# Kernel optimization log

Hardware: AMD Instinct MI355X
Metric: run time of the kernel (lower is better)

Reference implementation:

```python
import jax, jax.numpy as jnp
import numpy as np

N, E, C_IN, C_H, HOPS = 100000, 1600000, 10, 128, 3
LN_EPS = 1e-5


def setup_inputs() -> dict:
    key = jax.random.key(0)
    ks = jax.random.split(key, 8)
    s = 0.05  # weight init scale
    return {
        "x": jax.random.normal(ks[0], (N, C_IN), dtype=jnp.float32),
        "W_in": jax.random.normal(ks[1], (C_H, C_IN), dtype=jnp.float32) * s,
        "b_in": jnp.zeros((C_H,), jnp.float32),
        "hop_W": jax.random.normal(ks[2], (HOPS, C_H, C_H), dtype=jnp.float32) * s,
        "hop_b": jnp.zeros((HOPS, C_H), jnp.float32),
        "hop_g": jnp.ones((HOPS, C_H), jnp.float32),
        "hop_be": jnp.zeros((HOPS, C_H), jnp.float32),
        "gates": jax.random.normal(ks[3], (HOPS, C_H), dtype=jnp.float32),
        "fW": jax.random.normal(ks[4], (C_H, C_H), dtype=jnp.float32) * s,
        "fb": jnp.zeros((C_H,), jnp.float32),
        "fg": jnp.ones((C_H,), jnp.float32),
        "fbe": jnp.zeros((C_H,), jnp.float32),
        "edge_index": jax.random.randint(ks[5], (2, E), 0, N, dtype=jnp.int64) if jax.config.jax_enable_x64 else jax.random.randint(ks[5], (2, E), 0, N).astype(jnp.int32),
        "edge_attr": jax.random.randint(ks[6], (E,), 0, 5).astype(jnp.int32),
    }


def _layernorm(h, g, b):
    mu = h.mean(-1, keepdims=True)
    var = ((h - mu) ** 2).mean(-1, keepdims=True)  # biased var (torch LayerNorm)
    return (h - mu) * jax.lax.rsqrt(var + LN_EPS) * g + b


def _mpnn(x, src, dst, W, b, g, be):
    # ResidualMPNNLayer: scatter-max aggregate of x[src] at dst, linear, LN, residual relu.
    # dst entries equal to n act as a dummy bucket (for masked-out edges).
    n = x.shape[0]
    agg = jax.ops.segment_max(x[src], dst, num_segments=n + 1)[:n]
    # nodes with no incoming messages: torch_scatter fills with 0
    agg = jnp.where(jnp.isfinite(agg), agg, 0.0)
    return jax.nn.relu(_layernorm(agg @ W.T + b, g, be) + x)


def reference(x, W_in, b_in, hop_W, hop_b, hop_g, hop_be, gates, fW, fb, fg, fbe, edge_index, edge_attr):
    src, dst = edge_index[0], edge_index[1]
    n = x.shape[0]

    # ThreeHopSmallBlock
    h = jax.nn.relu(x @ W_in.T + b_in)  # [N, C_H]
    hop_outs = []
    for i in range(HOPS):
        h = _mpnn(h, src, dst, hop_W[i], hop_b[i], hop_g[i], hop_be[i])
        hop_outs.append(h)
    node_features = sum(o * jax.nn.sigmoid(gates[i]) for i, o in enumerate(hop_outs))
    # dropout inactive at inference

    # polygon subgraph: edges with attr == 3; masked edges scatter to dummy bucket n
    poly = edge_attr == 3
    dst_p = jnp.where(poly, dst, n)
    sub = _mpnn(node_features, src, dst_p, fW, fb, fg, fbe)  # [N, C_H]

    neg_inf = jnp.float32(-jnp.inf)
    fill = jnp.float32(1e-4)

    # sink nodes = unique destinations of polygon edges
    sink_mask = jax.ops.segment_sum(poly.astype(jnp.int32), dst, num_segments=n) > 0
    v2 = jnp.max(jnp.where(sink_mask[:, None], sub, neg_inf), axis=0, keepdims=True)
    v2 = jnp.where(jnp.any(sink_mask), v2, fill)

    # remaining nodes: NOT (x[:,0] > 0.1)
    rem = ~(x[:, 0] > 0.1)
    v3 = jnp.max(jnp.where(rem[:, None], node_features, neg_inf), axis=0, keepdims=True)
    v3 = jnp.where(jnp.any(rem), v3, fill)

    return jnp.concatenate([v2, v3], axis=0)  # [2, C_H]
```

## Files before the change

### kernel.cpp

```cpp
#include <hip/hip_runtime.h>
#include <hip/hip_bf16.h>
#include <cstdint>

#define N_NODES 100000
#define N_EDGES 1600000
#define C_IN    10
#define C_H     128
#define LN_EPS  1e-5f

#define SCAN_BLOCKS 98

__global__ void hist_kernel(const int* __restrict__ dst, const int* __restrict__ attr,
                            int* __restrict__ cnt, int* __restrict__ pcnt) {
    int i = blockIdx.x * blockDim.x + threadIdx.x;
    int stride = gridDim.x * blockDim.x;
    for (; i < N_EDGES; i += stride) {
        int d = dst[i];
        atomicAdd(&cnt[d], 1);
        if (attr[i] == 3) atomicAdd(&pcnt[d], 1);
    }
}

__device__ inline int wave_incl_scan(int v, int lane) {
#pragma unroll
    for (int off = 1; off < 64; off <<= 1) {
        int n = __shfl_up(v, off);
        if (lane >= off) v += n;
    }
    return v;
}

__global__ __launch_bounds__(1024) void scan1_kernel(const int* __restrict__ cnt,
                                                     int* __restrict__ excl,
                                                     int* __restrict__ bsum) {
    __shared__ int wsum[16];
    const int t = threadIdx.x, lane = t & 63, wid = t >> 6;
    const int i = blockIdx.x * 1024 + t;
    const int v = (i < N_NODES) ? cnt[i] : 0;
    int inc = wave_incl_scan(v, lane);
    if (lane == 63) wsum[wid] = inc;
    __syncthreads();
    if (t < 16) {
        int w = wsum[t];
#pragma unroll
        for (int off = 1; off < 16; off <<= 1) {
            int n = __shfl_up(w, off);
            if (t >= off) w += n;
        }
        wsum[t] = w;
    }
    __syncthreads();
    const int woff = (wid == 0) ? 0 : wsum[wid - 1];
    if (i < N_NODES) excl[i] = inc - v + woff;
    if (t == 0) bsum[blockIdx.x] = wsum[15];
}

__global__ void scan2_kernel(const int* __restrict__ bsum, int* __restrict__ bofs) {
    __shared__ int wsum[2];
    const int t = threadIdx.x, lane = t & 63, wid = t >> 6;
    const int v = (t < SCAN_BLOCKS) ? bsum[t] : 0;
    int inc = wave_incl_scan(v, lane);
    if (lane == 63) wsum[wid] = inc;
    __syncthreads();
    const int woff = (wid == 0) ? 0 : wsum[0];
    if (t < SCAN_BLOCKS) bofs[t] = inc - v + woff;
}

__global__ __launch_bounds__(1024) void scan3_kernel(const int* __restrict__ excl,
                                                     const int* __restrict__ bofs,
                                                     const int* __restrict__ pcnt,
                                                     int* __restrict__ row_off,
                                                     int* __restrict__ poly_end) {
    const int i = blockIdx.x * 1024 + threadIdx.x;
    if (i < N_NODES) {
        const int r = excl[i] + bofs[blockIdx.x];
        row_off[i]  = r;
        poly_end[i] = r + pcnt[i];
    }
    if (i == 0) row_off[N_NODES] = N_EDGES;
}

__global__ void scatter_kernel(const int* __restrict__ src, const int* __restrict__ dst,
                               const int* __restrict__ attr,
                               const int* __restrict__ row_off, const int* __restrict__ poly_end,
                               int* __restrict__ curP, int* __restrict__ curR,
                               int* __restrict__ pack) {
    int i = blockIdx.x * blockDim.x + threadIdx.x;
    int stride = gridDim.x * blockDim.x;
    for (; i < N_EDGES; i += stride) {
        int d = dst[i];
        int pos;
        if (attr[i] == 3) pos = row_off[d]  + atomicAdd(&curP[d], 1);
        else              pos = poly_end[d] + atomicAdd(&curR[d], 1);
        pack[pos] = src[i];
    }
}

__global__ void in_proj_kernel(const float* __restrict__ x, const float* __restrict__ Win,
                               const float* __restrict__ bin, float* __restrict__ h0) {
    __shared__ float Wl[C_H * 11];
    for (int i = threadIdx.x; i < C_H * C_IN; i += blockDim.x) {
        int c = i / C_IN, k = i % C_IN;
        Wl[c * 11 + k] = Win[i];
    }
    __syncthreads();
    const int l = threadIdx.x & 63, wid = threadIdx.x >> 6;
    const int wave = blockIdx.x * 4 + wid, nw = gridDim.x * 4;
    const float b0 = bin[l], b1 = bin[l + 64];
    for (int n = wave; n < N_NODES; n += nw) {
        float xr[C_IN];
#pragma unroll
        for (int k = 0; k < C_IN; ++k) xr[k] = x[n * C_IN + k];
        float a0 = b0, a1 = b1;
#pragma unroll
        for (int k = 0; k < C_IN; ++k) {
            a0 = fmaf(xr[k], Wl[l * 11 + k], a0);
            a1 = fmaf(xr[k], Wl[(l + 64) * 11 + k], a1);
        }
        h0[(size_t)n * C_H + l]      = fmaxf(a0, 0.f);
        h0[(size_t)n * C_H + l + 64] = fmaxf(a1, 0.f);
    }
}

#define NPW 4
#define LWAVES 16

template <int MODE>
__global__ __launch_bounds__(1024) void layer_kernel(
    const float* __restrict__ hin, float* __restrict__ hout,
    float* __restrict__ nf, const float* __restrict__ x,
    const int* __restrict__ row_off, const int* __restrict__ poly_end,
    const int* __restrict__ pack,
    const float* __restrict__ W, const float* __restrict__ bias,
    const float* __restrict__ gamma, const float* __restrict__ beta,
    const float* __restrict__ gate, float* __restrict__ out)
{
    __shared__ float Wl[C_H * 129];
    __shared__ float aggL[LWAVES][NPW * C_H];

    for (int i = threadIdx.x; i < C_H * C_H; i += 1024) {
        int c = i >> 7, k = i & 127;
        Wl[c * 129 + k] = W[i];
    }
    __syncthreads();

    const int l = threadIdx.x & 63, wid = threadIdx.x >> 6;
    const int wave = blockIdx.x * LWAVES + wid, nw = gridDim.x * LWAVES;

    const float b0 = bias[l],  b1 = bias[l + 64];
    const float g0 = gamma[l], g1 = gamma[l + 64];
    const float e0 = beta[l],  e1 = beta[l + 64];
    float sg0 = 0.f, sg1 = 0.f;
    if (MODE <= 2) {
        sg0 = 1.f / (1.f + expf(-gate[l]));
        sg1 = 1.f / (1.f + expf(-gate[l + 64]));
    }

    float red0 = 0.f, red1 = 0.f;

    const float* __restrict__ hb = hin + 2 * l;

    for (int base = wave * NPW; base < N_NODES; base += nw * NPW) {
        bool anyp[NPW];
        for (int j = 0; j < NPW; ++j) {
            const int n = base + j;
            float a0 = 0.f, a1 = 0.f;
            bool ap = false;
            if (n < N_NODES) {
                const int beg = row_off[n];
                const int end = (MODE == 3) ? poly_end[n] : row_off[n + 1];
                ap = (end > beg);
                int e = beg;
                for (; e + 8 <= end; e += 8) {
                    float2 v[8];
#pragma unroll
                    for (int t = 0; t < 8; ++t)
                        v[t] = *reinterpret_cast<const float2*>(hb + (size_t)pack[e + t] * C_H);
#pragma unroll
                    for (int t = 0; t < 8; ++t) {
                        a0 = fmaxf(a0, v[t].x);
                        a1 = fmaxf(a1, v[t].y);
                    }
                }
                for (; e + 2 <= end; e += 2) {
                    const float2 v0 = *reinterpret_cast<const float2*>(hb + (size_t)pack[e] * C_H);
                    const float2 v1 = *reinterpret_cast<const float2*>(hb + (size_t)pack[e + 1] * C_H);
                    a0 = fmaxf(a0, v0.x); a1 = fmaxf(a1, v0.y);
                    a0 = fmaxf(a0, v1.x); a1 = fmaxf(a1, v1.y);
                }
                if (e < end) {
                    const float2 v0 = *reinterpret_cast<const float2*>(hb + (size_t)pack[e] * C_H);
                    a0 = fmaxf(a0, v0.x); a1 = fmaxf(a1, v0.y);
                }
            }
            anyp[j] = ap;
            *reinterpret_cast<float2*>(&aggL[wid][j * C_H + 2 * l]) = make_float2(a0, a1);
        }

        float acc[NPW][2];
#pragma unroll
        for (int j = 0; j < NPW; ++j) { acc[j][0] = 0.f; acc[j][1] = 0.f; }
#pragma unroll 4
        for (int k = 0; k < C_H; ++k) {
            const float w0 = Wl[l * 129 + k];
            const float w1 = Wl[(l + 64) * 129 + k];
#pragma unroll
            for (int j = 0; j < NPW; ++j) {
                const float a = aggL[wid][j * C_H + k];
                acc[j][0] = fmaf(a, w0, acc[j][0]);
                acc[j][1] = fmaf(a, w1, acc[j][1]);
            }
        }

#pragma unroll
        for (int j = 0; j < NPW; ++j) {
            const int n = base + j;
            if (n < N_NODES) {
                float h0 = acc[j][0] + b0, h1 = acc[j][1] + b1;
                float s = h0 + h1, q = h0 * h0 + h1 * h1;
#pragma unroll
                for (int m = 1; m < 64; m <<= 1) {
                    s += __shfl_xor(s, m);
                    q += __shfl_xor(q, m);
                }
                const float mu  = s * (1.f / 128.f);
                const float var = q * (1.f / 128.f) - mu * mu;
                const float rs  = rsqrtf(var + LN_EPS);
                const float r0 = hin[(size_t)n * C_H + l];
                const float r1 = hin[(size_t)n * C_H + l + 64];
                const float o0 = fmaxf((h0 - mu) * rs * g0 + e0 + r0, 0.f);
                const float o1 = fmaxf((h1 - mu) * rs * g1 + e1 + r1, 0.f);
                if (MODE <= 1) {
                    hout[(size_t)n * C_H + l]      = o0;
                    hout[(size_t)n * C_H + l + 64] = o1;
                }
                if (MODE == 0) {
                    nf[(size_t)n * C_H + l]      = o0 * sg0;
                    nf[(size_t)n * C_H + l + 64] = o1 * sg1;
                } else if (MODE == 1) {
                    nf[(size_t)n * C_H + l]      += o0 * sg0;
                    nf[(size_t)n * C_H + l + 64] += o1 * sg1;
                } else if (MODE == 2) {
                    const float f0 = nf[(size_t)n * C_H + l]      + o0 * sg0;
                    const float f1 = nf[(size_t)n * C_H + l + 64] + o1 * sg1;
                    nf[(size_t)n * C_H + l]      = f0;
                    nf[(size_t)n * C_H + l + 64] = f1;
                    if (x[(size_t)n * C_IN] <= 0.1f) {
                        red0 = fmaxf(red0, f0);
                        red1 = fmaxf(red1, f1);
                    }
                } else {
                    if (anyp[j]) {
                        red0 = fmaxf(red0, o0);
                        red1 = fmaxf(red1, o1);
                    }
                }
            }
        }
    }

    if (MODE >= 2) {
        __syncthreads();
        float* red = &aggL[0][0];
        red[wid * 128 + l]      = red0;
        red[wid * 128 + 64 + l] = red1;
        __syncthreads();
        if (threadIdx.x < 128) {
            const int c = threadIdx.x;
            float m = red[c];
#pragma unroll
            for (int w = 1; w < LWAVES; ++w) m = fmaxf(m, red[w * 128 + c]);
            float* o = out + (MODE == 3 ? 0 : 128);
            atomicMax(reinterpret_cast<int*>(o + c), __float_as_int(m));
        }
    }
}

extern "C" void kernel_launch(void* const* d_in, const int* in_sizes, int n_in,
                              void* d_out, int out_size, void* d_ws, size_t ws_size,
                              hipStream_t stream) {
    const float* x      = (const float*)d_in[0];
    const float* W_in   = (const float*)d_in[1];
    const float* b_in   = (const float*)d_in[2];
    const float* hop_W  = (const float*)d_in[3];
    const float* hop_b  = (const float*)d_in[4];
    const float* hop_g  = (const float*)d_in[5];
    const float* hop_be = (const float*)d_in[6];
    const float* gates  = (const float*)d_in[7];
    const float* fW     = (const float*)d_in[8];
    const float* fb     = (const float*)d_in[9];
    const float* fg     = (const float*)d_in[10];
    const float* fbe    = (const float*)d_in[11];
    const int*   eidx   = (const int*)d_in[12];
    const int*   eattr  = (const int*)d_in[13];
    float* out = (float*)d_out;

    char* ws = (char*)d_ws;
    size_t off = 0;
    auto alloc = [&](size_t bytes) {
        char* p = ws + off;
        off = (off + bytes + 255) & ~(size_t)255;
        return p;
    };
    int*   cnt      = (int*)alloc((size_t)N_NODES * 4);
    int*   pcnt     = (int*)alloc((size_t)N_NODES * 4);
    int*   curP     = (int*)alloc((size_t)N_NODES * 4);
    int*   curR     = (int*)alloc((size_t)N_NODES * 4);
    int*   excl     = (int*)alloc((size_t)N_NODES * 4);
    int*   bsum     = (int*)alloc((size_t)SCAN_BLOCKS * 4);
    int*   bofs     = (int*)alloc((size_t)SCAN_BLOCKS * 4);
    int*   row_off  = (int*)alloc((size_t)(N_NODES + 1) * 4);
    int*   polyend  = (int*)alloc((size_t)N_NODES * 4);
    int*   pack     = (int*)alloc((size_t)N_EDGES * 4);
    float* hA       = (float*)alloc((size_t)N_NODES * C_H * 4);
    float* hB       = (float*)alloc((size_t)N_NODES * C_H * 4);
    float* nf       = (float*)alloc((size_t)N_NODES * C_H * 4);
    (void)ws_size;

    const int* src = eidx;
    const int* dst = eidx + N_EDGES;

    hipMemsetAsync(cnt,  0, (size_t)N_NODES * 4, stream);
    hipMemsetAsync(pcnt, 0, (size_t)N_NODES * 4, stream);
    hipMemsetAsync(curP, 0, (size_t)N_NODES * 4, stream);
    hipMemsetAsync(curR, 0, (size_t)N_NODES * 4, stream);
    hipMemsetAsync(d_out, 0, 256 * 4, stream);

    hist_kernel<<<2048, 256, 0, stream>>>(dst, eattr, cnt, pcnt);
    scan1_kernel<<<SCAN_BLOCKS, 1024, 0, stream>>>(cnt, excl, bsum);
    scan2_kernel<<<1, 128, 0, stream>>>(bsum, bofs);
    scan3_kernel<<<SCAN_BLOCKS, 1024, 0, stream>>>(excl, bofs, pcnt, row_off, polyend);
    scatter_kernel<<<2048, 256, 0, stream>>>(src, dst, eattr, row_off, polyend, curP, curR, pack);
    in_proj_kernel<<<2048, 256, 0, stream>>>(x, W_in, b_in, hA);

    layer_kernel<0><<<256, 1024, 0, stream>>>(hA, hB, nf, x, row_off, polyend, pack,
                                              hop_W + 0 * C_H * C_H, hop_b + 0 * C_H,
                                              hop_g + 0 * C_H, hop_be + 0 * C_H,
                                              gates + 0 * C_H, out);
    layer_kernel<1><<<256, 1024, 0, stream>>>(hB, hA, nf, x, row_off, polyend, pack,
                                              hop_W + 1 * C_H * C_H, hop_b + 1 * C_H,
                                              hop_g + 1 * C_H, hop_be + 1 * C_H,
                                              gates + 1 * C_H, out);
    layer_kernel<2><<<256, 1024, 0, stream>>>(hA, nullptr, nf, x, row_off, polyend, pack,
                                              hop_W + 2 * C_H * C_H, hop_b + 2 * C_H,
                                              hop_g + 2 * C_H, hop_be + 2 * C_H,
                                              gates + 2 * C_H, out);
    layer_kernel<3><<<256, 1024, 0, stream>>>(nf, nullptr, nullptr, x, row_off, polyend, pack,
                                              fW, fb, fg, fbe, nullptr, out);
}
```

Measured before the change: 812.3 us.

## Split wave into half-waves gathering float4 rows, raise nodes per wave

The edge gather is restructured so each half-wave handles alternate edges and each lane loads a float4 (4 channels) rather than a float2, with the two halves merged by a cross-lane shuffle max. This halves the serial gather loop length per node and widens the loads, targeting gather memory latency. Nodes per wave rises from 4 to 8 to amortize the LDS matvec, and the residual loads are hoisted ahead of the matvec so they overlap it. The costs are more register pressure from the larger accumulator and residual arrays, plus extra shuffles.

```diff
diff --git a/kernel.cpp b/kernel.cpp
--- a/kernel.cpp
+++ b/kernel.cpp
@@ -122,8 +122,23 @@
     }
 }
 
-#define NPW 4
+#define NPW 8
 #define LWAVES 16
+
+#define GATHER_BLOCK(NB)                                                       \
+    for (; e + 2 * NB <= end; e += 2 * NB) {                                   \
+        float4 v[NB];                                                          \
+        _Pragma("unroll")                                                      \
+        for (int t = 0; t < NB; ++t) {                                         \
+            const int s = pack[e + 2 * t + half];                              \
+            v[t] = *reinterpret_cast<const float4*>(hq + ((size_t)s << 7));    \
+        }                                                                      \
+        _Pragma("unroll")                                                      \
+        for (int t = 0; t < NB; ++t) {                                         \
+            a0 = fmaxf(a0, v[t].x); a1 = fmaxf(a1, v[t].y);                    \
+            a2 = fmaxf(a2, v[t].z); a3 = fmaxf(a3, v[t].w);                    \
+        }                                                                      \
+    }
 
 template <int MODE>
 __global__ __launch_bounds__(1024) void layer_kernel(
@@ -145,6 +160,8 @@
     __syncthreads();
 
     const int l = threadIdx.x & 63, wid = threadIdx.x >> 6;
+    const int half = l >> 5;
+    const int q4 = (l & 31) << 2;
     const int wave = blockIdx.x * LWAVES + wid, nw = gridDim.x * LWAVES;
 
     const float b0 = bias[l],  b1 = bias[l + 64];
@@ -158,43 +175,47 @@
 
     float red0 = 0.f, red1 = 0.f;
 
-    const float* __restrict__ hb = hin + 2 * l;
+    const float* __restrict__ hq = hin + q4;
 
     for (int base = wave * NPW; base < N_NODES; base += nw * NPW) {
         bool anyp[NPW];
         for (int j = 0; j < NPW; ++j) {
             const int n = base + j;
-            float a0 = 0.f, a1 = 0.f;
+            float a0 = 0.f, a1 = 0.f, a2 = 0.f, a3 = 0.f;
             bool ap = false;
             if (n < N_NODES) {
                 const int beg = row_off[n];
                 const int end = (MODE == 3) ? poly_end[n] : row_off[n + 1];
                 ap = (end > beg);
                 int e = beg;
-                for (; e + 8 <= end; e += 8) {
-                    float2 v[8];
-#pragma unroll
-                    for (int t = 0; t < 8; ++t)
-                        v[t] = *reinterpret_cast<const float2*>(hb + (size_t)pack[e + t] * C_H);
-#pragma unroll
-                    for (int t = 0; t < 8; ++t) {
-                        a0 = fmaxf(a0, v[t].x);
-                        a1 = fmaxf(a1, v[t].y);
-                    }
-                }
-                for (; e + 2 <= end; e += 2) {
-                    const float2 v0 = *reinterpret_cast<const float2*>(hb + (size_t)pack[e] * C_H);
-                    const float2 v1 = *reinterpret_cast<const float2*>(hb + (size_t)pack[e + 1] * C_H);
-                    a0 = fmaxf(a0, v0.x); a1 = fmaxf(a1, v0.y);
-                    a0 = fmaxf(a0, v1.x); a1 = fmaxf(a1, v1.y);
-                }
+                GATHER_BLOCK(8)
+                GATHER_BLOCK(4)
+                GATHER_BLOCK(2)
+                GATHER_BLOCK(1)
                 if (e < end) {
-                    const float2 v0 = *reinterpret_cast<const float2*>(hb + (size_t)pack[e] * C_H);
-                    a0 = fmaxf(a0, v0.x); a1 = fmaxf(a1, v0.y);
+                    const int s = pack[e];
+                    const float4 v = *reinterpret_cast<const float4*>(hq + ((size_t)s << 7));
+                    a0 = fmaxf(a0, v.x); a1 = fmaxf(a1, v.y);
+                    a2 = fmaxf(a2, v.z); a3 = fmaxf(a3, v.w);
                 }
             }
+            a0 = fmaxf(a0, __shfl_xor(a0, 32));
+            a1 = fmaxf(a1, __shfl_xor(a1, 32));
+            a2 = fmaxf(a2, __shfl_xor(a2, 32));
+            a3 = fmaxf(a3, __shfl_xor(a3, 32));
             anyp[j] = ap;
-            *reinterpret_cast<float2*>(&aggL[wid][j * C_H + 2 * l]) = make_float2(a0, a1);
+            if (half == 0)
+                *reinterpret_cast<float4*>(&aggL[wid][j * C_H + q4]) = make_float4(a0, a1, a2, a3);
+        }
+
+        float r0v[NPW], r1v[NPW];
+#pragma unroll
+        for (int j = 0; j < NPW; ++j) {
+            const int n = base + j;
+            if (n < N_NODES) {
+                r0v[j] = hin[(size_t)n * C_H + l];
+                r1v[j] = hin[(size_t)n * C_H + l + 64];
+            }
         }
 
         float acc[NPW][2];
@@ -226,10 +247,8 @@
                 const float mu  = s * (1.f / 128.f);
                 const float var = q * (1.f / 128.f) - mu * mu;
                 const float rs  = rsqrtf(var + LN_EPS);
-                const float r0 = hin[(size_t)n * C_H + l];
-                const float r1 = hin[(size_t)n * C_H + l + 64];
-                const float o0 = fmaxf((h0 - mu) * rs * g0 + e0 + r0, 0.f);
-                const float o1 = fmaxf((h1 - mu) * rs * g1 + e1 + r1, 0.f);
+                const float o0 = fmaxf((h0 - mu) * rs * g0 + e0 + r0v[j], 0.f);
+                const float o1 = fmaxf((h1 - mu) * rs * g1 + e1 + r1v[j], 0.f);
                 if (MODE <= 1) {
                     hout[(size_t)n * C_H + l]      = o0;
                     hout[(size_t)n * C_H + l + 64] = o1;
```

New measurement: 867.2 us. 6.8% more time.

## Replace LDS aggregate staging with wave shuffles, raise occupancy and grid size

Applied to the files above, without the earlier changes.

Each wave's per-node max-aggregates now stay in registers and are broadcast with __shfl inside the 128x128 matvec, instead of being staged in a per-wave shared-memory buffer. Dropping that buffer shrinks the block's LDS use so more blocks can fit per CU, and the layer grid doubles from 256 to 512 blocks with a stricter launch bound. The gather loop adds a 4-edge unrolled tail, and the four counter memsets are merged into one contiguous memset. The tighter launch bound caps registers and may cause spills, and a shuffle per element per k may cost about as much as the LDS reads it replaces.

```diff
diff --git a/kernel.cpp b/kernel.cpp
--- a/kernel.cpp
+++ b/kernel.cpp
@@ -126,7 +126,7 @@
 #define LWAVES 16
 
 template <int MODE>
-__global__ __launch_bounds__(1024) void layer_kernel(
+__global__ __launch_bounds__(1024, 8) void layer_kernel(
     const float* __restrict__ hin, float* __restrict__ hout,
     float* __restrict__ nf, const float* __restrict__ x,
     const int* __restrict__ row_off, const int* __restrict__ poly_end,
@@ -136,7 +136,7 @@
     const float* __restrict__ gate, float* __restrict__ out)
 {
     __shared__ float Wl[C_H * 129];
-    __shared__ float aggL[LWAVES][NPW * C_H];
+    __shared__ float red[LWAVES * C_H];
 
     for (int i = threadIdx.x; i < C_H * C_H; i += 1024) {
         int c = i >> 7, k = i & 127;
@@ -162,9 +162,11 @@
 
     for (int base = wave * NPW; base < N_NODES; base += nw * NPW) {
         bool anyp[NPW];
+        float a0[NPW], a1[NPW];
+#pragma unroll
         for (int j = 0; j < NPW; ++j) {
             const int n = base + j;
-            float a0 = 0.f, a1 = 0.f;
+            float p0 = 0.f, p1 = 0.f;
             bool ap = false;
             if (n < N_NODES) {
                 const int beg = row_off[n];
@@ -178,23 +180,30 @@
                         v[t] = *reinterpret_cast<const float2*>(hb + (size_t)pack[e + t] * C_H);
 #pragma unroll
                     for (int t = 0; t < 8; ++t) {
-                        a0 = fmaxf(a0, v[t].x);
-                        a1 = fmaxf(a1, v[t].y);
+                        p0 = fmaxf(p0, v[t].x); p1 = fmaxf(p1, v[t].y);
                     }
                 }
+                for (; e + 4 <= end; e += 4) {
+                    const float2 v0 = *reinterpret_cast<const float2*>(hb + (size_t)pack[e]     * C_H);
+                    const float2 v1 = *reinterpret_cast<const float2*>(hb + (size_t)pack[e + 1] * C_H);
+                    const float2 v2 = *reinterpret_cast<const float2*>(hb + (size_t)pack[e + 2] * C_H);
+                    const float2 v3 = *reinterpret_cast<const float2*>(hb + (size_t)pack[e + 3] * C_H);
+                    p0 = fmaxf(p0, fmaxf(fmaxf(v0.x, v1.x), fmaxf(v2.x, v3.x)));
+                    p1 = fmaxf(p1, fmaxf(fmaxf(v0.y, v1.y), fmaxf(v2.y, v3.y)));
+                }
                 for (; e + 2 <= end; e += 2) {
-                    const float2 v0 = *reinterpret_cast<const float2*>(hb + (size_t)pack[e] * C_H);
+                    const float2 v0 = *reinterpret_cast<const float2*>(hb + (size_t)pack[e]     * C_H);
                     const float2 v1 = *reinterpret_cast<const float2*>(hb + (size_t)pack[e + 1] * C_H);
-                    a0 = fmaxf(a0, v0.x); a1 = fmaxf(a1, v0.y);
-                    a0 = fmaxf(a0, v1.x); a1 = fmaxf(a1, v1.y);
+                    p0 = fmaxf(p0, fmaxf(v0.x, v1.x));
+                    p1 = fmaxf(p1, fmaxf(v0.y, v1.y));
                 }
                 if (e < end) {
                     const float2 v0 = *reinterpret_cast<const float2*>(hb + (size_t)pack[e] * C_H);
-                    a0 = fmaxf(a0, v0.x); a1 = fmaxf(a1, v0.y);
+                    p0 = fmaxf(p0, v0.x); p1 = fmaxf(p1, v0.y);
                 }
             }
             anyp[j] = ap;
-            *reinterpret_cast<float2*>(&aggL[wid][j * C_H + 2 * l]) = make_float2(a0, a1);
+            a0[j] = p0; a1[j] = p1;
         }
 
         float acc[NPW][2];
@@ -204,9 +213,10 @@
         for (int k = 0; k < C_H; ++k) {
             const float w0 = Wl[l * 129 + k];
             const float w1 = Wl[(l + 64) * 129 + k];
+            const int sl = k >> 1;
 #pragma unroll
             for (int j = 0; j < NPW; ++j) {
-                const float a = aggL[wid][j * C_H + k];
+                const float a = __shfl((k & 1) ? a1[j] : a0[j], sl);
                 acc[j][0] = fmaf(a, w0, acc[j][0]);
                 acc[j][1] = fmaf(a, w1, acc[j][1]);
             }
@@ -261,7 +271,6 @@
 
     if (MODE >= 2) {
         __syncthreads();
-        float* red = &aggL[0][0];
         red[wid * 128 + l]      = red0;
         red[wid * 128 + 64 + l] = red1;
         __syncthreads();
@@ -302,6 +311,7 @@
         off = (off + bytes + 255) & ~(size_t)255;
         return p;
     };
+    const size_t npad = ((size_t)N_NODES * 4 + 255) & ~(size_t)255;
     int*   cnt      = (int*)alloc((size_t)N_NODES * 4);
     int*   pcnt     = (int*)alloc((size_t)N_NODES * 4);
     int*   curP     = (int*)alloc((size_t)N_NODES * 4);
@@ -320,10 +330,7 @@
     const int* src = eidx;
     const int* dst = eidx + N_EDGES;
 
-    hipMemsetAsync(cnt,  0, (size_t)N_NODES * 4, stream);
-    hipMemsetAsync(pcnt, 0, (size_t)N_NODES * 4, stream);
-    hipMemsetAsync(curP, 0, (size_t)N_NODES * 4, stream);
-    hipMemsetAsync(curR, 0, (size_t)N_NODES * 4, stream);
+    hipMemsetAsync(cnt, 0, npad * 4, stream);
     hipMemsetAsync(d_out, 0, 256 * 4, stream);
 
     hist_kernel<<<2048, 256, 0, stream>>>(dst, eattr, cnt, pcnt);
@@ -333,18 +340,18 @@
     scatter_kernel<<<2048, 256, 0, stream>>>(src, dst, eattr, row_off, polyend, curP, curR, pack);
     in_proj_kernel<<<2048, 256, 0, stream>>>(x, W_in, b_in, hA);
 
-    layer_kernel<0><<<256, 1024, 0, stream>>>(hA, hB, nf, x, row_off, polyend, pack,
+    layer_kernel<0><<<512, 1024, 0, stream>>>(hA, hB, nf, x, row_off, polyend, pack,
                                               hop_W + 0 * C_H * C_H, hop_b + 0 * C_H,
                                               hop_g + 0 * C_H, hop_be + 0 * C_H,
                                               gates + 0 * C_H, out);
-    layer_kernel<1><<<256, 1024, 0, stream>>>(hB, hA, nf, x, row_off, polyend, pack,
+    layer_kernel<1><<<512, 1024, 0, stream>>>(hB, hA, nf, x, row_off, polyend, pack,
                                               hop_W + 1 * C_H * C_H, hop_b + 1 * C_H,
                                               hop_g + 1 * C_H, hop_be + 1 * C_H,
                                               gates + 1 * C_H, out);
-    layer_kernel<2><<<256, 1024, 0, stream>>>(hA, nullptr, nf, x, row_off, polyend, pack,
+    layer_kernel<2><<<512, 1024, 0, stream>>>(hA, nullptr, nf, x, row_off, polyend, pack,
                                               hop_W + 2 * C_H * C_H, hop_b + 2 * C_H,
                                               hop_g + 2 * C_H, hop_be + 2 * C_H,
                                               gates + 2 * C_H, out);
-    layer_kernel<3><<<256, 1024, 0, stream>>>(nf, nullptr, nullptr, x, row_off, polyend, pack,
+    layer_kernel<3><<<512, 1024, 0, stream>>>(nf, nullptr, nullptr, x, row_off, polyend, pack,
                                               fW, fb, fg, fbe, nullptr, out);
 }
```

Result: slower. 1.131 ms (+39.3%).
